# Optimization experiments

Measured on AMD Instinct MI355X. Metric: run time of the kernel, lower is better.

The kernel has to match this reference:

```python
import jax, jax.numpy as jnp
import numpy as np


def setup_inputs() -> dict:
    key = jax.random.key(0)
    k1, k2, k3 = jax.random.split(key, 3)
    B, T, C = 16, 8192, 256
    inputs = jax.random.normal(k1, (B, T, C), dtype=jnp.float32)
    initial_state = jax.random.normal(k2, (B, C), dtype=jnp.float32)
    # learned smoothing coeff, per-channel, init'd near coeff_init=0.1
    smooth = jax.random.uniform(k3, (C,), dtype=jnp.float32)
    return {"inputs": inputs, "initial_state": initial_state, "smooth": smooth}


def reference(inputs, initial_state, smooth):
    """EMA recurrence y_t = w*x_t + (1-w)*y_{t-1}, vectorized via associative scan.

    inputs: [B, T, C], initial_state: [B, C], smooth: [C].
    The linear recurrence y_t = a*y_{t-1} + b_t (a = 1-w, b_t = w*x_t) is
    computed in O(log T) depth with lax.associative_scan over pairs (a, b),
    composing (a1,b1) then (a2,b2) -> (a1*a2, a2*b1 + b2). The initial state
    is folded in afterwards: y_t = A_t * y_0 + B_t.
    """
    w = jnp.clip(smooth, 0.0, 1.0)                      # [C]
    a = jnp.broadcast_to(1.0 - w, inputs.shape)         # [B, T, C]
    b = w * inputs                                      # [B, T, C]

    def combine(c1, c2):
        a1, b1 = c1
        a2, b2 = c2
        return a1 * a2, a2 * b1 + b2

    A, Bc = jax.lax.associative_scan(combine, (a, b), axis=1)
    return A * initial_state[:, None, :] + Bc           # [B, T, C]
```

## Files before the change

kernel.cpp:

```cpp
#include <hip/hip_runtime.h>


#define CHUNK_L 64
#define SENTI64 0xFFFFFFFFFFFFFFFFull

__device__ __forceinline__ float clip01(float v) {
    return fminf(fmaxf(v, 0.0f), 1.0f);
}

__global__ __launch_bounds__(64) void ema_fused(
    const float* __restrict__ x, const float* __restrict__ smooth,
    const float* __restrict__ init, float* __restrict__ out,
    float* __restrict__ chunk_last, unsigned int* __restrict__ flags,
    int T, int C, int P) {
    const int blk = blockIdx.x;
    const int b = blk / P;
    const int p = blk - b * P;
    const int t = threadIdx.x;
    const int c = t << 2;

    float4 w4 = *(const float4*)(smooth + c);
    w4.x = clip01(w4.x); w4.y = clip01(w4.y); w4.z = clip01(w4.z); w4.w = clip01(w4.w);
    const float ax = 1.0f - w4.x, ay = 1.0f - w4.y, az = 1.0f - w4.z, aw = 1.0f - w4.w;

    const int sF4 = C >> 2;
    const size_t base = ((size_t)b * T + (size_t)p * CHUNK_L) * C;
    const float4* xp = (const float4*)(x + base) + t;

    float y0 = 0.0f, y1 = 0.0f, y2 = 0.0f, y3 = 0.0f;
    for (int i0 = 0; i0 < CHUNK_L; i0 += 8) {
        float4 xv[8];
#pragma unroll
        for (int j = 0; j < 8; ++j) xv[j] = xp[(size_t)(i0 + j) * sF4];
#pragma unroll
        for (int j = 0; j < 8; ++j) {
            y0 = fmaf(ax, y0, w4.x * xv[j].x);
            y1 = fmaf(ay, y1, w4.y * xv[j].y);
            y2 = fmaf(az, y2, w4.z * xv[j].z);
            y3 = fmaf(aw, y3, w4.w * xv[j].w);
        }
    }
    {
        union { float f[4]; unsigned long long u[2]; } r;
        r.f[0] = y0; r.f[1] = y1; r.f[2] = y2; r.f[3] = y3;
        unsigned long long* dst =
            (unsigned long long*)(chunk_last + (size_t)blk * C + c);
        __hip_atomic_store(dst + 0, r.u[0], __ATOMIC_RELAXED, __HIP_MEMORY_SCOPE_AGENT);
        __hip_atomic_store(dst + 1, r.u[1], __ATOMIC_RELAXED, __HIP_MEMORY_SCOPE_AGENT);
    }
    asm volatile("s_waitcnt vmcnt(0)" ::: "memory");
    if (t == 0) {
        __hip_atomic_store(flags + blk, 1u, __ATOMIC_RELAXED, __HIP_MEMORY_SCOPE_AGENT);
    }

    float aLx = ax, aLy = ay, aLz = az, aLw = aw;
    for (int e = CHUNK_L; e > 1; e >>= 1) { aLx *= aLx; aLy *= aLy; aLz *= aLz; aLw *= aLw; }

    float4 s = *(const float4*)(init + (size_t)b * C + c);
    if (p > 0) {
        const unsigned int* fl = flags + (size_t)b * P;
        const unsigned long long* cl =
            (const unsigned long long*)(chunk_last + (size_t)b * P * C) + (t << 1);
        const int sU64 = C >> 1;

        int q = 0;
        for (; q + 8 <= p; q += 8) {
            while (__hip_atomic_load(fl + (q + 7), __ATOMIC_RELAXED,
                                     __HIP_MEMORY_SCOPE_AGENT) == 0u) {
                __builtin_amdgcn_s_sleep(16);
            }
            union { float f[4]; unsigned long long u[2]; } l[8];
            for (;;) {
                bool ok = true;
#pragma unroll
                for (int j = 0; j < 8; ++j) {
                    const unsigned long long* src = cl + (size_t)(q + j) * sU64;
                    l[j].u[0] = __hip_atomic_load(src + 0, __ATOMIC_RELAXED,
                                                  __HIP_MEMORY_SCOPE_AGENT);
                    l[j].u[1] = __hip_atomic_load(src + 1, __ATOMIC_RELAXED,
                                                  __HIP_MEMORY_SCOPE_AGENT);
                    ok &= (l[j].u[0] != SENTI64) & (l[j].u[1] != SENTI64);
                }
                if (__all((int)ok)) break;
                __builtin_amdgcn_s_sleep(2);
            }
#pragma unroll
            for (int j = 0; j < 8; ++j) {
                s.x = fmaf(aLx, s.x, l[j].f[0]);
                s.y = fmaf(aLy, s.y, l[j].f[1]);
                s.z = fmaf(aLz, s.z, l[j].f[2]);
                s.w = fmaf(aLw, s.w, l[j].f[3]);
            }
        }
        for (; q < p; ++q) {
            while (__hip_atomic_load(fl + q, __ATOMIC_RELAXED,
                                     __HIP_MEMORY_SCOPE_AGENT) == 0u) {
                __builtin_amdgcn_s_sleep(8);
            }
            union { float f[4]; unsigned long long u[2]; } l;
            const unsigned long long* src = cl + (size_t)q * sU64;
            for (;;) {
                l.u[0] = __hip_atomic_load(src + 0, __ATOMIC_RELAXED,
                                           __HIP_MEMORY_SCOPE_AGENT);
                l.u[1] = __hip_atomic_load(src + 1, __ATOMIC_RELAXED,
                                           __HIP_MEMORY_SCOPE_AGENT);
                if (__all((int)((l.u[0] != SENTI64) & (l.u[1] != SENTI64)))) break;
                __builtin_amdgcn_s_sleep(2);
            }
            s.x = fmaf(aLx, s.x, l.f[0]);
            s.y = fmaf(aLy, s.y, l.f[1]);
            s.z = fmaf(aLz, s.z, l.f[2]);
            s.w = fmaf(aLw, s.w, l.f[3]);
        }
    }

    float4* op = (float4*)(out + base) + t;
    float yb0 = s.x, yb1 = s.y, yb2 = s.z, yb3 = s.w;
    for (int i0 = 0; i0 < CHUNK_L; i0 += 8) {
        float4 xv[8];
#pragma unroll
        for (int j = 0; j < 8; ++j) xv[j] = xp[(size_t)(i0 + j) * sF4];
#pragma unroll
        for (int j = 0; j < 8; ++j) {
            yb0 = fmaf(ax, yb0, w4.x * xv[j].x);
            yb1 = fmaf(ay, yb1, w4.y * xv[j].y);
            yb2 = fmaf(az, yb2, w4.z * xv[j].z);
            yb3 = fmaf(aw, yb3, w4.w * xv[j].w);
            float4 r; r.x = yb0; r.y = yb1; r.z = yb2; r.w = yb3;
            op[(size_t)(i0 + j) * sF4] = r;
        }
    }
}

extern "C" void kernel_launch(void* const* d_in, const int* in_sizes, int n_in,
                              void* d_out, int out_size, void* d_ws, size_t ws_size,
                              hipStream_t stream) {
    const float* x      = (const float*)d_in[0];
    const float* init   = (const float*)d_in[1];
    const float* smooth = (const float*)d_in[2];
    float* out = (float*)d_out;

    const int C  = in_sizes[2];
    const int BC = in_sizes[1];
    const int B  = BC / C;
    const int T  = in_sizes[0] / BC;
    const int P  = T / CHUNK_L;

    float* chunk_last = (float*)d_ws;
    unsigned int* flags =
        (unsigned int*)((char*)d_ws + (size_t)B * P * C * sizeof(float));

    (void)hipMemsetAsync(chunk_last, 0xFF, (size_t)B * P * C * sizeof(float), stream);
    (void)hipMemsetAsync(flags, 0, (size_t)B * P * sizeof(unsigned int), stream);

    ema_fused<<<dim3(B * P), dim3(C / 4), 0, stream>>>(
        x, smooth, init, out, chunk_last, flags, T, C, P);
}
```

Before: 278.3 us.

## Split chunk across four waves, keep inputs in registers, add ticket-ordered block IDs

Each 64-step chunk is now handled by four wavefronts of 16 steps each. Each wave computes a local aggregate, and the aggregates are combined through shared memory. The input tile is kept in registers, so x is read only once instead of twice. Block IDs come from an atomic ticket counter, so predecessor chunks are guaranteed to be scheduled first, which avoids deadlock and reduces spin waiting in the decoupled look-back. Wave 0 alone does the serial look-back while the other waves wait at a barrier, and register pressure rises from holding 16 float4 values per thread.

Result: faster. 266.2 us (-4.4%).

```diff
diff --git a/kernel.cpp b/kernel.cpp
--- a/kernel.cpp
+++ b/kernel.cpp
@@ -2,133 +2,170 @@
 
 
 #define CHUNK_L 64
+#define SUB 16
+#define NW 4
 #define SENTI64 0xFFFFFFFFFFFFFFFFull
 
 __device__ __forceinline__ float clip01(float v) {
     return fminf(fmaxf(v, 0.0f), 1.0f);
 }
 
-__global__ __launch_bounds__(64) void ema_fused(
+__global__ __launch_bounds__(256) void ema_fused(
     const float* __restrict__ x, const float* __restrict__ smooth,
     const float* __restrict__ init, float* __restrict__ out,
     float* __restrict__ chunk_last, unsigned int* __restrict__ flags,
-    int T, int C, int P) {
-    const int blk = blockIdx.x;
+    unsigned int* __restrict__ ticket, int T, int C, int P) {
+    __shared__ unsigned int vblk_sh;
+    __shared__ float agg_sh[NW][256];
+    __shared__ float seed_sh[256];
+
+    const int tid = threadIdx.x;
+    const int wv  = tid >> 6;
+    const int ln  = tid & 63;
+    const int c   = ln << 2;
+
+    if (tid == 0) vblk_sh = atomicAdd(ticket, 1u);
+    __syncthreads();
+    const int blk = (int)vblk_sh;
     const int b = blk / P;
     const int p = blk - b * P;
-    const int t = threadIdx.x;
-    const int c = t << 2;
 
     float4 w4 = *(const float4*)(smooth + c);
     w4.x = clip01(w4.x); w4.y = clip01(w4.y); w4.z = clip01(w4.z); w4.w = clip01(w4.w);
     const float ax = 1.0f - w4.x, ay = 1.0f - w4.y, az = 1.0f - w4.z, aw = 1.0f - w4.w;
 
+    float aSx = ax, aSy = ay, aSz = az, aSw = aw;
+    for (int e = SUB; e > 1; e >>= 1) { aSx *= aSx; aSy *= aSy; aSz *= aSz; aSw *= aSw; }
+    float aLx = aSx, aLy = aSy, aLz = aSz, aLw = aSw;
+    for (int e = CHUNK_L / SUB; e > 1; e >>= 1) { aLx *= aLx; aLy *= aLy; aLz *= aLz; aLw *= aLw; }
+
     const int sF4 = C >> 2;
-    const size_t base = ((size_t)b * T + (size_t)p * CHUNK_L) * C;
-    const float4* xp = (const float4*)(x + base) + t;
+    const size_t base =
+        ((size_t)b * T + (size_t)p * CHUNK_L + (size_t)wv * SUB) * C;
+    const float4* xp = (const float4*)(x + base) + ln;
+
+    float4 xv[SUB];
+#pragma unroll
+    for (int j = 0; j < SUB; ++j) xv[j] = xp[(size_t)j * sF4];
 
     float y0 = 0.0f, y1 = 0.0f, y2 = 0.0f, y3 = 0.0f;
-    for (int i0 = 0; i0 < CHUNK_L; i0 += 8) {
-        float4 xv[8];
 #pragma unroll
-        for (int j = 0; j < 8; ++j) xv[j] = xp[(size_t)(i0 + j) * sF4];
+    for (int j = 0; j < SUB; ++j) {
+        y0 = fmaf(ax, y0, w4.x * xv[j].x);
+        y1 = fmaf(ay, y1, w4.y * xv[j].y);
+        y2 = fmaf(az, y2, w4.z * xv[j].z);
+        y3 = fmaf(aw, y3, w4.w * xv[j].w);
+    }
+    { float4 r; r.x = y0; r.y = y1; r.z = y2; r.w = y3;
+      *(float4*)&agg_sh[wv][c] = r; }
+    __syncthreads();
+
+    if (wv == 0) {
+        float4 g = *(const float4*)&agg_sh[0][c];
 #pragma unroll
-        for (int j = 0; j < 8; ++j) {
-            y0 = fmaf(ax, y0, w4.x * xv[j].x);
-            y1 = fmaf(ay, y1, w4.y * xv[j].y);
-            y2 = fmaf(az, y2, w4.z * xv[j].z);
-            y3 = fmaf(aw, y3, w4.w * xv[j].w);
+        for (int v = 1; v < NW; ++v) {
+            const float4 av = *(const float4*)&agg_sh[v][c];
+            g.x = fmaf(aSx, g.x, av.x);
+            g.y = fmaf(aSy, g.y, av.y);
+            g.z = fmaf(aSz, g.z, av.z);
+            g.w = fmaf(aSw, g.w, av.w);
         }
-    }
-    {
-        union { float f[4]; unsigned long long u[2]; } r;
-        r.f[0] = y0; r.f[1] = y1; r.f[2] = y2; r.f[3] = y3;
-        unsigned long long* dst =
-            (unsigned long long*)(chunk_last + (size_t)blk * C + c);
-        __hip_atomic_store(dst + 0, r.u[0], __ATOMIC_RELAXED, __HIP_MEMORY_SCOPE_AGENT);
-        __hip_atomic_store(dst + 1, r.u[1], __ATOMIC_RELAXED, __HIP_MEMORY_SCOPE_AGENT);
-    }
-    asm volatile("s_waitcnt vmcnt(0)" ::: "memory");
-    if (t == 0) {
-        __hip_atomic_store(flags + blk, 1u, __ATOMIC_RELAXED, __HIP_MEMORY_SCOPE_AGENT);
-    }
+        {
+            union { float f[4]; unsigned long long u[2]; } r;
+            r.f[0] = g.x; r.f[1] = g.y; r.f[2] = g.z; r.f[3] = g.w;
+            unsigned long long* dst =
+                (unsigned long long*)(chunk_last + (size_t)blk * C + c);
+            __hip_atomic_store(dst + 0, r.u[0], __ATOMIC_RELAXED, __HIP_MEMORY_SCOPE_AGENT);
+            __hip_atomic_store(dst + 1, r.u[1], __ATOMIC_RELAXED, __HIP_MEMORY_SCOPE_AGENT);
+        }
+        asm volatile("s_waitcnt vmcnt(0)" ::: "memory");
+        if (ln == 0) {
+            __hip_atomic_store(flags + blk, 1u, __ATOMIC_RELAXED, __HIP_MEMORY_SCOPE_AGENT);
+        }
 
-    float aLx = ax, aLy = ay, aLz = az, aLw = aw;
-    for (int e = CHUNK_L; e > 1; e >>= 1) { aLx *= aLx; aLy *= aLy; aLz *= aLz; aLw *= aLw; }
+        float4 s = *(const float4*)(init + (size_t)b * C + c);
+        if (p > 0) {
+            const unsigned int* fl = flags + (size_t)b * P;
+            const unsigned long long* cl =
+                (const unsigned long long*)(chunk_last + (size_t)b * P * C) + (ln << 1);
+            const int sU64 = C >> 1;
 
-    float4 s = *(const float4*)(init + (size_t)b * C + c);
-    if (p > 0) {
-        const unsigned int* fl = flags + (size_t)b * P;
-        const unsigned long long* cl =
-            (const unsigned long long*)(chunk_last + (size_t)b * P * C) + (t << 1);
-        const int sU64 = C >> 1;
-
-        int q = 0;
-        for (; q + 8 <= p; q += 8) {
-            while (__hip_atomic_load(fl + (q + 7), __ATOMIC_RELAXED,
-                                     __HIP_MEMORY_SCOPE_AGENT) == 0u) {
-                __builtin_amdgcn_s_sleep(16);
-            }
-            union { float f[4]; unsigned long long u[2]; } l[8];
-            for (;;) {
-                bool ok = true;
+            int q = 0;
+            for (; q + 8 <= p; q += 8) {
+                while (__hip_atomic_load(fl + (q + 7), __ATOMIC_RELAXED,
+                                         __HIP_MEMORY_SCOPE_AGENT) == 0u) {
+                    __builtin_amdgcn_s_sleep(16);
+                }
+                union { float f[4]; unsigned long long u[2]; } l[8];
+                for (;;) {
+                    bool ok = true;
+#pragma unroll
+                    for (int j = 0; j < 8; ++j) {
+                        const unsigned long long* src = cl + (size_t)(q + j) * sU64;
+                        l[j].u[0] = __hip_atomic_load(src + 0, __ATOMIC_RELAXED,
+                                                      __HIP_MEMORY_SCOPE_AGENT);
+                        l[j].u[1] = __hip_atomic_load(src + 1, __ATOMIC_RELAXED,
+                                                      __HIP_MEMORY_SCOPE_AGENT);
+                        ok &= (l[j].u[0] != SENTI64) & (l[j].u[1] != SENTI64);
+                    }
+                    if (__all((int)ok)) break;
+                    __builtin_amdgcn_s_sleep(2);
+                }
 #pragma unroll
                 for (int j = 0; j < 8; ++j) {
-                    const unsigned long long* src = cl + (size_t)(q + j) * sU64;
-                    l[j].u[0] = __hip_atomic_load(src + 0, __ATOMIC_RELAXED,
-                                                  __HIP_MEMORY_SCOPE_AGENT);
-                    l[j].u[1] = __hip_atomic_load(src + 1, __ATOMIC_RELAXED,
-                                                  __HIP_MEMORY_SCOPE_AGENT);
-                    ok &= (l[j].u[0] != SENTI64) & (l[j].u[1] != SENTI64);
+                    s.x = fmaf(aLx, s.x, l[j].f[0]);
+                    s.y = fmaf(aLy, s.y, l[j].f[1]);
+                    s.z = fmaf(aLz, s.z, l[j].f[2]);
+                    s.w = fmaf(aLw, s.w, l[j].f[3]);
                 }
-                if (__all((int)ok)) break;
-                __builtin_amdgcn_s_sleep(2);
             }
-#pragma unroll
-            for (int j = 0; j < 8; ++j) {
-                s.x = fmaf(aLx, s.x, l[j].f[0]);
-                s.y = fmaf(aLy, s.y, l[j].f[1]);
-                s.z = fmaf(aLz, s.z, l[j].f[2]);
-                s.w = fmaf(aLw, s.w, l[j].f[3]);
+            for (; q < p; ++q) {
+                while (__hip_atomic_load(fl + q, __ATOMIC_RELAXED,
+                                         __HIP_MEMORY_SCOPE_AGENT) == 0u) {
+                    __builtin_amdgcn_s_sleep(8);
+                }
+                union { float f[4]; unsigned long long u[2]; } l;
+                const unsigned long long* src = cl + (size_t)q * sU64;
+                for (;;) {
+                    l.u[0] = __hip_atomic_load(src + 0, __ATOMIC_RELAXED,
+                                               __HIP_MEMORY_SCOPE_AGENT);
+                    l.u[1] = __hip_atomic_load(src + 1, __ATOMIC_RELAXED,
+                                               __HIP_MEMORY_SCOPE_AGENT);
+                    if (__all((int)((l.u[0] != SENTI64) & (l.u[1] != SENTI64)))) break;
+                    __builtin_amdgcn_s_sleep(2);
+                }
+                s.x = fmaf(aLx, s.x, l.f[0]);
+                s.y = fmaf(aLy, s.y, l.f[1]);
+                s.z = fmaf(aLz, s.z, l.f[2]);
+                s.w = fmaf(aLw, s.w, l.f[3]);
             }
         }
-        for (; q < p; ++q) {
-            while (__hip_atomic_load(fl + q, __ATOMIC_RELAXED,
-                                     __HIP_MEMORY_SCOPE_AGENT) == 0u) {
-                __builtin_amdgcn_s_sleep(8);
-            }
-            union { float f[4]; unsigned long long u[2]; } l;
-            const unsigned long long* src = cl + (size_t)q * sU64;
-            for (;;) {
-                l.u[0] = __hip_atomic_load(src + 0, __ATOMIC_RELAXED,
-                                           __HIP_MEMORY_SCOPE_AGENT);
-                l.u[1] = __hip_atomic_load(src + 1, __ATOMIC_RELAXED,
-                                           __HIP_MEMORY_SCOPE_AGENT);
-                if (__all((int)((l.u[0] != SENTI64) & (l.u[1] != SENTI64)))) break;
-                __builtin_amdgcn_s_sleep(2);
-            }
-            s.x = fmaf(aLx, s.x, l.f[0]);
-            s.y = fmaf(aLy, s.y, l.f[1]);
-            s.z = fmaf(aLz, s.z, l.f[2]);
-            s.w = fmaf(aLw, s.w, l.f[3]);
+        *(float4*)&seed_sh[c] = s;
+    }
+    __syncthreads();
+
+    float4 sd = *(const float4*)&seed_sh[c];
+#pragma unroll
+    for (int v = 0; v < NW - 1; ++v) {
+        if (v < wv) {
+            const float4 av = *(const float4*)&agg_sh[v][c];
+            sd.x = fmaf(aSx, sd.x, av.x);
+            sd.y = fmaf(aSy, sd.y, av.y);
+            sd.z = fmaf(aSz, sd.z, av.z);
+            sd.w = fmaf(aSw, sd.w, av.w);
         }
     }
 
-    float4* op = (float4*)(out + base) + t;
-    float yb0 = s.x, yb1 = s.y, yb2 = s.z, yb3 = s.w;
-    for (int i0 = 0; i0 < CHUNK_L; i0 += 8) {
-        float4 xv[8];
+    float4* op = (float4*)(out + base) + ln;
+    float yb0 = sd.x, yb1 = sd.y, yb2 = sd.z, yb3 = sd.w;
 #pragma unroll
-        for (int j = 0; j < 8; ++j) xv[j] = xp[(size_t)(i0 + j) * sF4];
-#pragma unroll
-        for (int j = 0; j < 8; ++j) {
-            yb0 = fmaf(ax, yb0, w4.x * xv[j].x);
-            yb1 = fmaf(ay, yb1, w4.y * xv[j].y);
-            yb2 = fmaf(az, yb2, w4.z * xv[j].z);
-            yb3 = fmaf(aw, yb3, w4.w * xv[j].w);
-            float4 r; r.x = yb0; r.y = yb1; r.z = yb2; r.w = yb3;
-            op[(size_t)(i0 + j) * sF4] = r;
-        }
+    for (int j = 0; j < SUB; ++j) {
+        yb0 = fmaf(ax, yb0, w4.x * xv[j].x);
+        yb1 = fmaf(ay, yb1, w4.y * xv[j].y);
+        yb2 = fmaf(az, yb2, w4.z * xv[j].z);
+        yb3 = fmaf(aw, yb3, w4.w * xv[j].w);
+        float4 r; r.x = yb0; r.y = yb1; r.z = yb2; r.w = yb3;
+        op[(size_t)j * sF4] = r;
     }
 }
 
@@ -149,10 +186,11 @@
     float* chunk_last = (float*)d_ws;
     unsigned int* flags =
         (unsigned int*)((char*)d_ws + (size_t)B * P * C * sizeof(float));
+    unsigned int* ticket = flags + (size_t)B * P;
 
     (void)hipMemsetAsync(chunk_last, 0xFF, (size_t)B * P * C * sizeof(float), stream);
-    (void)hipMemsetAsync(flags, 0, (size_t)B * P * sizeof(unsigned int), stream);
+    (void)hipMemsetAsync(flags, 0, ((size_t)B * P + 1) * sizeof(unsigned int), stream);
 
-    ema_fused<<<dim3(B * P), dim3(C / 4), 0, stream>>>(
-        x, smooth, init, out, chunk_last, flags, T, C, P);
+    ema_fused<<<dim3(B * P), dim3(NW * 64), 0, stream>>>(
+        x, smooth, init, out, chunk_last, flags, ticket, T, C, P);
 }
```
